# Kernel tuning notes

Measured on AMD Instinct MI355X. Metric: run time of the kernel, lower is better.

Reference implementation:

```python
import jax, jax.numpy as jnp
import numpy as np

CHAR_EMB = 30
CHAR_HID = 100  # bidirectional -> 50 per direction
HID = CHAR_HID // 2
VOCAB = 100
B, S, T = 64, 256, 16


def setup_inputs() -> dict:
    key = jax.random.key(0)
    ks = jax.random.split(key, 10)
    char_ids = jax.random.randint(ks[0], (B, S, T), 0, VOCAB, dtype=jnp.int64)
    scale = np.sqrt(3.0 / CHAR_EMB)
    emb = jax.random.uniform(ks[1], (VOCAB, CHAR_EMB), minval=-scale, maxval=scale, dtype=jnp.float32)
    # torch LSTM param layout: w_ih [4H, in], w_hh [4H, H], gate order i,f,g,o
    k = 1.0 / np.sqrt(HID)
    def u(kk, shape):
        return jax.random.uniform(kk, shape, minval=-k, maxval=k, dtype=jnp.float32)
    return {
        "char_ids": char_ids,
        "emb": emb,
        "w_ih_f": u(ks[2], (4 * HID, CHAR_EMB)), "w_hh_f": u(ks[3], (4 * HID, HID)),
        "b_ih_f": u(ks[4], (4 * HID,)), "b_hh_f": u(ks[5], (4 * HID,)),
        "w_ih_r": u(ks[6], (4 * HID, CHAR_EMB)), "w_hh_r": u(ks[7], (4 * HID, HID)),
        "b_ih_r": u(ks[8], (4 * HID,)), "b_hh_r": u(ks[9], (4 * HID,)),
    }


def _lstm_scan(x, w_ih, w_hh, b_ih, b_hh):
    # x: [N, T, E] -> outputs ys [T, N, H], final h [N, H]
    N = x.shape[0]
    xw = jnp.einsum('nte,ge->ntg', x, w_ih) + (b_ih + b_hh)  # [N, T, 4H]
    xw = jnp.transpose(xw, (1, 0, 2))  # [T, N, 4H]

    def step(carry, xt):
        h, c = carry
        gates = xt + h @ w_hh.T
        i, f, g, o = jnp.split(gates, 4, axis=-1)
        i = jax.nn.sigmoid(i); f = jax.nn.sigmoid(f)
        g = jnp.tanh(g); o = jax.nn.sigmoid(o)
        c = f * c + i * g
        h = o * jnp.tanh(c)
        return (h, c), h

    h0 = jnp.zeros((N, HID), x.dtype)
    (hT, _), ys = jax.lax.scan(step, (h0, h0), xw)
    return ys, hT


def reference(char_ids, emb, w_ih_f, w_hh_f, b_ih_f, b_hh_f,
              w_ih_r, w_hh_r, b_ih_r, b_hh_r):
    b, s, t = char_ids.shape
    ids = char_ids.reshape(b * s, t)                 # [N, T]
    lengths = (ids != 0).sum(axis=1)                 # ragged lengths (pad id 0)
    x = emb[ids]                                     # [N, T, E]; dropout = identity (eval)

    # forward direction: need hidden at position lengths-1
    ys_f, _ = _lstm_scan(x, w_ih_f, w_hh_f, b_ih_f, b_hh_f)   # [T, N, H]
    ys_f = jnp.transpose(ys_f, (1, 0, 2))                      # [N, T, H]
    idx = jnp.maximum(lengths - 1, 0)[:, None, None]           # guard all-pad rows
    h_fwd = jnp.take_along_axis(ys_f, idx, axis=1)[:, 0, :]    # [N, H]

    # backward direction: output at t=0 == final carry of reversed scan
    _, h_bwd = _lstm_scan(x[:, ::-1, :], w_ih_r, w_hh_r, b_ih_r, b_hh_r)  # [N, H]

    out = jnp.concatenate([h_fwd, h_bwd], axis=-1)   # [N, 2H]
    return out.reshape(b, s, CHAR_HID)
```

## Files before the change

kernel.cpp:

```cpp
#include <hip/hip_runtime.h>

#define T 16
#define E 30
#define H 50
#define VOCAB 100
#define ROWS 208
#define K1 1.44269504089f
#define K2 2.88539008178f
#define NTILE 13

typedef _Float16 v8hf __attribute__((ext_vector_type(8)));
typedef float v4f __attribute__((ext_vector_type(4)));

extern "C" __device__ float __ocml_native_exp2_f32(float);
__device__ __forceinline__ float e2(float x)   { return __ocml_native_exp2_f32(x); }
__device__ __forceinline__ float rcpf(float x) { return __builtin_amdgcn_rcpf(x); }

__global__ void build_tbl(const float* __restrict__ emb,
                          const float* __restrict__ w_ih,
                          const float* __restrict__ b_ih,
                          const float* __restrict__ b_hh,
                          float* __restrict__ tbl) {
    int idx = blockIdx.x * blockDim.x + threadIdx.x;
    if (idx >= VOCAB * ROWS) return;
    int v = idx / ROWS, r = idx % ROWS;
    int tile = r >> 4, rho = r & 15;
    int lgc = rho >> 2, gate = rho & 3;
    int u = lgc * 13 + tile;
    float s = 0.f;
    if (u < H) {
        int orig = gate * H + u;
        s = b_ih[orig] + b_hh[orig];
        const float* er = emb + v * E;
        const float* wr = w_ih + orig * E;
#pragma unroll
        for (int e = 0; e < E; ++e) s += er[e] * wr[e];
        s *= (gate == 2) ? K2 : -K1;
    }
    tbl[idx] = s;
}

__global__ __launch_bounds__(256, 2) void lstm_mfma(
    const int* __restrict__ ids,
    const float* __restrict__ tbl,
    const float* __restrict__ whh_f,
    const float* __restrict__ whh_r,
    float* __restrict__ out)
{
    const int tid = threadIdx.x;
    const int lane = tid & 63;
    const int wave = tid >> 6;
    const int l15 = lane & 15;
    const int lg = lane >> 4;
    const int b = blockIdx.x;
    const int dir = b >> 8;
    const int seq = (b & 255) * 64 + wave * 16 + l15;

    const float* __restrict__ whh = dir ? whh_r : whh_f;
    const float* __restrict__ tb  = tbl + dir * (VOCAB * ROWS);
    const int* __restrict__ myids = ids + seq * T;

    int capt;
    {
        const int4* q = (const int4*)myids;
        int4 a0 = q[0], a1 = q[1], a2 = q[2], a3 = q[3];
        int len = (a0.x != 0) + (a0.y != 0) + (a0.z != 0) + (a0.w != 0)
                + (a1.x != 0) + (a1.y != 0) + (a1.z != 0) + (a1.w != 0)
                + (a2.x != 0) + (a2.y != 0) + (a2.z != 0) + (a2.w != 0)
                + (a3.x != 0) + (a3.y != 0) + (a3.z != 0) + (a3.w != 0);
        capt = dir ? (T - 1) : ((len > 1) ? (len - 1) : 0);
    }

    const int gate = l15 & 3;
    const int rbase = (l15 >> 2) * 13;
    const float sc = (gate == 2) ? K2 : -K1;
    v8hf afrag[NTILE][2];
#pragma unroll
    for (int i = 0; i < NTILE; ++i) {
        const int urow = rbase + i;
        const bool vrow = (urow < H);
        const int worow = (gate * H + (vrow ? urow : 0)) * H;
#pragma unroll
        for (int kh = 0; kh < 2; ++kh) {
            v8hf af;
#pragma unroll
            for (int j = 0; j < 8; ++j) {
                const int m = kh * 8 + j;
                const int ucol = lg * 13 + m;
                const bool vcol = (m < NTILE) && (ucol < H);
                af[j] = (_Float16)((vrow && vcol) ? sc * whh[worow + ucol] : 0.f);
            }
            afrag[i][kh] = af;
        }
    }

    float cs[NTILE];
#pragma unroll
    for (int i = 0; i < NTILE; ++i) cs[i] = 0.f;

    v8hf b0 = (v8hf)(_Float16)0.f;
    v8hf b1 = (v8hf)(_Float16)0.f;

    v4f tv[NTILE];
    {
        const int id0 = myids[dir ? (T - 1) : 0];
        const float* __restrict__ trow = tb + id0 * ROWS;
#pragma unroll
        for (int i = 0; i < NTILE; ++i)
            tv[i] = *(const v4f*)(trow + i * 16 + lg * 4);
    }

#pragma unroll 1
    for (int t = 0; t < T; ++t) {
        int tn = dir ? (T - 2 - t) : (t + 1);
        if (t == T - 1) tn = dir ? 0 : (T - 1);
        const int id_next = myids[tn];
        const float* __restrict__ trow_n = tb + id_next * ROWS;
        const bool cap = (t == capt);

        float hn[NTILE];
#pragma unroll
        for (int i = 0; i < NTILE; ++i) {
            v4f c = __builtin_amdgcn_mfma_f32_16x16x32_f16(afrag[i][0], b0, tv[i], 0, 0, 0);
            c = __builtin_amdgcn_mfma_f32_16x16x32_f16(afrag[i][1], b1, c, 0, 0, 0);
            tv[i] = *(const v4f*)(trow_n + i * 16 + lg * 4);

            float ei = e2(c[0]);
            float ef = e2(c[1]);
            float eg = e2(c[2]);
            float eo = e2(c[3]);
            float ai  = 1.f + ei;
            float bf  = 1.f + ef;
            float gp  = eg + 1.f;
            float gm2 = fmaf(K2, eg, -K2);
            float num = fmaf(cs[i] * ai, gp, gm2 * bf);
            float rD  = rcpf(ai * bf * gp);
            float cn  = num * rD;
            cs[i] = cn;
            float ec  = e2(cn);
            float h   = (ec - 1.f) * rcpf((1.f + eo) * (ec + 1.f));

            if (i >= 11) h = (lg < 3) ? h : 0.f;
            hn[i] = h;
            if (cap && (i < 11 || lg < 3))
                out[seq * 100 + dir * H + lg * NTILE + i] = h;
        }

        v8hf nb0, nb1;
#pragma unroll
        for (int j = 0; j < 8; ++j) nb0[j] = (_Float16)hn[j];
#pragma unroll
        for (int j = 0; j < 5; ++j) nb1[j] = (_Float16)hn[8 + j];
        nb1[5] = (_Float16)0.f; nb1[6] = (_Float16)0.f; nb1[7] = (_Float16)0.f;
        b0 = nb0; b1 = nb1;
    }
}

extern "C" void kernel_launch(void* const* d_in, const int* in_sizes, int n_in,
                              void* d_out, int out_size, void* d_ws, size_t ws_size,
                              hipStream_t stream) {
    const int*   char_ids = (const int*)d_in[0];
    const float* emb      = (const float*)d_in[1];
    const float* w_ih_f   = (const float*)d_in[2];
    const float* w_hh_f   = (const float*)d_in[3];
    const float* b_ih_f   = (const float*)d_in[4];
    const float* b_hh_f   = (const float*)d_in[5];
    const float* w_ih_r   = (const float*)d_in[6];
    const float* w_hh_r   = (const float*)d_in[7];
    const float* b_ih_r   = (const float*)d_in[8];
    const float* b_hh_r   = (const float*)d_in[9];
    float* out = (float*)d_out;
    float* tbl = (float*)d_ws;

    const int nt = VOCAB * ROWS;
    build_tbl<<<(nt + 255) / 256, 256, 0, stream>>>(emb, w_ih_f, b_ih_f, b_hh_f, tbl);
    build_tbl<<<(nt + 255) / 256, 256, 0, stream>>>(emb, w_ih_r, b_ih_r, b_hh_r, tbl + nt);
    lstm_mfma<<<512, 256, 0, stream>>>(char_ids, tbl, w_hh_f, w_hh_r, out);
}
```

Measured before the change: 66.10 us.

## Stage fp16 input-projection table in LDS instead of prefetching from global

Each block copies its direction's precomputed input-projection table into shared memory as fp16 with a padded row stride. Each timestep then reads its gate preactivations from LDS instead of prefetching them from global memory one step ahead. The goal is to take global-memory latency and register pressure off the recurrent loop. In exchange, every block pays an upfront copy of about 20K elements plus a barrier, the table loses precision by going to fp16, and the 42KB LDS footprint may limit occupancy. The lane masking for padding rows (i>=11) is also removed, on the assumption that the corresponding A columns are already zero.

```diff
diff --git a/kernel.cpp b/kernel.cpp
--- a/kernel.cpp
+++ b/kernel.cpp
@@ -8,8 +8,10 @@
 #define K1 1.44269504089f
 #define K2 2.88539008178f
 #define NTILE 13
+#define TSTRIDE 210
 
 typedef _Float16 v8hf __attribute__((ext_vector_type(8)));
+typedef _Float16 v4hf __attribute__((ext_vector_type(4)));
 typedef float v4f __attribute__((ext_vector_type(4)));
 
 extern "C" __device__ float __ocml_native_exp2_f32(float);
@@ -47,6 +49,8 @@
     const float* __restrict__ whh_r,
     float* __restrict__ out)
 {
+    __shared__ _Float16 tl[VOCAB * TSTRIDE];
+
     const int tid = threadIdx.x;
     const int lane = tid & 63;
     const int wave = tid >> 6;
@@ -59,6 +63,11 @@
     const float* __restrict__ whh = dir ? whh_r : whh_f;
     const float* __restrict__ tb  = tbl + dir * (VOCAB * ROWS);
     const int* __restrict__ myids = ids + seq * T;
+
+    for (int idx = tid; idx < VOCAB * ROWS; idx += 256) {
+        int v = idx / ROWS, r = idx - v * ROWS;
+        tl[v * TSTRIDE + r] = (_Float16)tb[idx];
+    }
 
     int capt;
     {
@@ -94,6 +103,8 @@
         }
     }
 
+    __syncthreads();
+
     float cs[NTILE];
 #pragma unroll
     for (int i = 0; i < NTILE; ++i) cs[i] = 0.f;
@@ -101,29 +112,30 @@
     v8hf b0 = (v8hf)(_Float16)0.f;
     v8hf b1 = (v8hf)(_Float16)0.f;
 
-    v4f tv[NTILE];
-    {
-        const int id0 = myids[dir ? (T - 1) : 0];
-        const float* __restrict__ trow = tb + id0 * ROWS;
-#pragma unroll
-        for (int i = 0; i < NTILE; ++i)
-            tv[i] = *(const v4f*)(trow + i * 16 + lg * 4);
-    }
+    int id_next = myids[dir ? (T - 1) : 0];
 
 #pragma unroll 1
     for (int t = 0; t < T; ++t) {
+        const int id = id_next;
         int tn = dir ? (T - 2 - t) : (t + 1);
         if (t == T - 1) tn = dir ? 0 : (T - 1);
-        const int id_next = myids[tn];
-        const float* __restrict__ trow_n = tb + id_next * ROWS;
+        id_next = myids[tn];
+
+        const _Float16* __restrict__ trow = tl + id * TSTRIDE + lg * 4;
         const bool cap = (t == capt);
 
-        float hn[NTILE];
+        v8hf nb0;
+        v8hf nb1 = (v8hf)(_Float16)0.f;
+
 #pragma unroll
         for (int i = 0; i < NTILE; ++i) {
-            v4f c = __builtin_amdgcn_mfma_f32_16x16x32_f16(afrag[i][0], b0, tv[i], 0, 0, 0);
+            v4hf th = *(const v4hf*)(trow + i * 16);
+            v4f tvv;
+            tvv[0] = (float)th[0]; tvv[1] = (float)th[1];
+            tvv[2] = (float)th[2]; tvv[3] = (float)th[3];
+
+            v4f c = __builtin_amdgcn_mfma_f32_16x16x32_f16(afrag[i][0], b0, tvv, 0, 0, 0);
             c = __builtin_amdgcn_mfma_f32_16x16x32_f16(afrag[i][1], b1, c, 0, 0, 0);
-            tv[i] = *(const v4f*)(trow_n + i * 16 + lg * 4);
 
             float ei = e2(c[0]);
             float ef = e2(c[1]);
@@ -140,18 +152,11 @@
             float ec  = e2(cn);
             float h   = (ec - 1.f) * rcpf((1.f + eo) * (ec + 1.f));
 
-            if (i >= 11) h = (lg < 3) ? h : 0.f;
-            hn[i] = h;
+            if (i < 8) nb0[i] = (_Float16)h;
+            else       nb1[i - 8] = (_Float16)h;
             if (cap && (i < 11 || lg < 3))
                 out[seq * 100 + dir * H + lg * NTILE + i] = h;
         }
-
-        v8hf nb0, nb1;
-#pragma unroll
-        for (int j = 0; j < 8; ++j) nb0[j] = (_Float16)hn[j];
-#pragma unroll
-        for (int j = 0; j < 5; ++j) nb1[j] = (_Float16)hn[8 + j];
-        nb1[5] = (_Float16)0.f; nb1[6] = (_Float16)0.f; nb1[7] = (_Float16)0.f;
         b0 = nb0; b1 = nb1;
     }
 }
```

Result: slower. 76.70 us (+16.0%).
